# Kernel tuning notes

Measured on AMD Instinct MI355X. Metric: run time of the kernel, lower is better.

## Reference

```python
import jax, jax.numpy as jnp
import numpy as np

C = 1024
T = 2048
B = 8

def setup_inputs() -> dict:
    key = jax.random.key(0)
    ks = jax.random.split(key, 7)
    s = lambda fan_in: 1.0 / np.sqrt(fan_in)
    return {
        "x":     jax.random.normal(ks[0], (B, T, C), dtype=jnp.float32),
        "w_qkv": jax.random.uniform(ks[1], (C, 3 * C), jnp.float32, -s(C), s(C)),
        "w_proj": jax.random.uniform(ks[2], (C, C), jnp.float32, -s(C), s(C)),
        "w1":    jax.random.uniform(ks[3], (C, 2 * C), jnp.float32, -s(C), s(C)),
        "w2":    jax.random.uniform(ks[4], (2 * C, C), jnp.float32, -s(2 * C), s(2 * C)),
        "g1":    jnp.ones((C,), jnp.float32),
        "g2":    jnp.ones((C,), jnp.float32),
    }

def rmsnorm(x, g, eps=1e-6):
    return x * jax.lax.rsqrt(jnp.mean(x * x, axis=-1, keepdims=True) + eps) * g

def reference(x, w_qkv, w_proj, w1, w2, g1, g2):
    t = x.shape[1]
    # --- attention ---
    h = rmsnorm(x, g1)
    qkv = h @ w_qkv                               # [B,T,3C]
    q, k, v = jnp.split(qkv, 3, axis=-1)
    scores = jnp.einsum('bqc,bkc->bqk', q, k) * (C ** -0.5)  # [B,T,T]
    causal = jnp.triu(jnp.ones((t, t), dtype=bool), k=1)
    scores = jnp.where(causal, -jnp.inf, scores)
    attn = jax.nn.softmax(scores, axis=-1)
    x = x + (attn @ v) @ w_proj
    # --- ffn ---
    h = rmsnorm(x, g2)
    return x + (jax.nn.silu(h @ w1)) @ w2
```

## Files before the change

kernel.cpp:

```cpp
#include <hip/hip_runtime.h>
#include <hip/hip_bf16.h>
#include <stdint.h>


#define C_DIM 1024
#define T_DIM 2048
#define B_DIM 8

typedef float f32x4 __attribute__((ext_vector_type(4)));
typedef __bf16 bf16x8 __attribute__((ext_vector_type(8)));

typedef const __attribute__((address_space(1))) void gvoid_t;
typedef __attribute__((address_space(3))) void lvoid_t;

__device__ __forceinline__ void gload_lds16(const void* g, void* l) {
    __builtin_amdgcn_global_load_lds((gvoid_t*)g, (lvoid_t*)l, 16, 0, 0);
}

__device__ __forceinline__ unsigned short f2bf_bits(float f) {
    __hip_bfloat16 h = __float2bfloat16(f);
    return *reinterpret_cast<unsigned short*>(&h);
}

__device__ __forceinline__ void xcd_remap(int& bx, int& by, int& bz) {
    const int gx = gridDim.x, gy = gridDim.y;
    const int nwg = gx * gy * (int)gridDim.z;
    const int orig = bx + gx * (by + gy * bz);
    const int q = nwg >> 3, r = nwg & 7;
    const int xcd = orig & 7, pos = orig >> 3;
    const int neu = (xcd < r ? xcd * (q + 1) : r * (q + 1) + (xcd - r) * q) + pos;
    bx = neu % gx;
    const int t = neu / gx;
    by = t % gy;
    bz = t / gy;
}

#define BAR() do { __builtin_amdgcn_s_barrier(); __builtin_amdgcn_sched_barrier(0); } while(0)
#define VMCNT(n) do { asm volatile("s_waitcnt vmcnt(" #n ")" ::: "memory"); \
                      __builtin_amdgcn_sched_barrier(0); } while(0)

#define RD_A(dst, buf, hq) do { \
    _Pragma("unroll") \
    for (int mf_ = 0; mf_ < 4; ++mf_) { \
        const char* p_ = lds + (buf)*32768 + wrb + (hq)*8192 + mf_*2048; \
        dst[mf_][0] = *(const bf16x8*)(p_ + offk0); \
        dst[mf_][1] = *(const bf16x8*)(p_ + offk1); \
    } \
} while(0)

#define RD_B(dst, buf, nh) do { \
    _Pragma("unroll") \
    for (int n2_ = 0; n2_ < 2; ++n2_) { \
        const char* p_ = lds + 65536 + (buf)*32768 + wcb + ((nh)*2 + n2_)*2048; \
        dst[n2_][0] = *(const bf16x8*)(p_ + offk0); \
        dst[n2_][1] = *(const bf16x8*)(p_ + offk1); \
    } \
} while(0)

#define MMQ(aS, bS, Mh, Nh) do { \
    __builtin_amdgcn_s_setprio(1); \
    _Pragma("unroll") \
    for (int m4_ = 0; m4_ < 4; ++m4_) \
    _Pragma("unroll") \
    for (int n2_ = 0; n2_ < 2; ++n2_) \
    _Pragma("unroll") \
    for (int ks_ = 0; ks_ < 2; ++ks_) \
        acc[(Mh)*4 + m4_][(Nh)*2 + n2_] = __builtin_amdgcn_mfma_f32_16x16x32_bf16( \
            aS[m4_][ks_], bS[n2_][ks_], acc[(Mh)*4 + m4_][(Nh)*2 + n2_], 0, 0, 0); \
    __builtin_amdgcn_s_setprio(0); \
} while(0)

#define STA(buf, half, kt) do { \
    const int go_ = aoff + (half)*128*lda + (kt)*64; \
    char* lp_ = ldsw + (buf)*32768 + (half)*16384; \
    gload_lds16(A + go_,            lp_); \
    gload_lds16(A + go_ + 64*lda,   lp_ + 8192); \
} while(0)
#define STB(buf, half, kt) do { \
    const int go_ = boff + (half)*128*ldb + (kt)*64; \
    char* lp_ = ldsw + 65536 + (buf)*32768 + (half)*16384; \
    gload_lds16(Bt + go_,           lp_); \
    gload_lds16(Bt + go_ + 64*ldb,  lp_ + 8192); \
} while(0)
#define STAGE4(buf, kt) do { STA(buf,0,kt); STA(buf,1,kt); STB(buf,0,kt); STB(buf,1,kt); } while(0)

template<int EPI, int CMODE>
__global__ __launch_bounds__(512, 2)
void gemm256(const __hip_bfloat16* A, const __hip_bfloat16* Bt,
             void* Cout, const float* R, void* C2, void* C3,
             int K, int lda, int ldb, int ldc,
             long long sA, long long sB, long long sC, float scale)
{
    int bx = blockIdx.x, by = blockIdx.y, bz = blockIdx.z;
    xcd_remap(bx, by, bz);
    if constexpr (CMODE == 1) { if (bx > by) return; }

    const int tid  = threadIdx.x;
    const int lane = tid & 63, wave = tid >> 6;
    const int l15  = lane & 15, l4 = lane >> 4;
    const int wr   = wave >> 2, wc = wave & 3;
    const int m0   = by * 256, n0 = bx * 256;
    const int z    = bz;

    A  += (long long)z * sA;
    Bt += (long long)z * sB;

    __shared__ __align__(16) char lds_[131072];
    char* lds  = lds_;
    char* ldsw = lds_ + wave * 1024;

    int kmax = K;
    if constexpr (CMODE == 2) { int km = m0 + 256; kmax = km < K ? km : K; }
    const int NT = kmax >> 6, niter = NT >> 1;

    const int offk0 = l15 * 128 + (((l4)     ^ (l15 & 7)) << 4);
    const int offk1 = l15 * 128 + (((4 + l4) ^ (l15 & 7)) << 4);
    const int wrb = wr * 16384, wcb = wc * 8192;

    const int rowq  = tid >> 3;
    const int sslot = (tid & 7) ^ (rowq & 7);
    const int aoff  = (m0 + rowq) * lda + sslot * 8;
    const int boff  = (n0 + rowq) * ldb + sslot * 8;

    f32x4 acc[8][4];
#pragma unroll
    for (int i = 0; i < 8; ++i)
#pragma unroll
        for (int j = 0; j < 4; ++j) acc[i][j] = (f32x4){0.f, 0.f, 0.f, 0.f};
    bf16x8 aP[4][2], aQ[4][2], bL[2][2], bH[2][2];

    STAGE4(0, 0);
    STAGE4(1, 1);
    VMCNT(8);
    BAR();
    RD_A(aP, 0, 0);
    RD_B(bL, 0, 0);

    for (int it = 0; it < niter; ++it) {
        const int t0 = 2 * it, t1 = 2 * it + 1;
        RD_B(bH, 0, 1);            MMQ(aP, bL, 0, 0);
        RD_A(aQ, 0, 1);            MMQ(aP, bH, 0, 1);
                                   MMQ(aQ, bL, 1, 0);
        VMCNT(0); BAR();
        if (t0 + 2 < NT) STAGE4(0, t0 + 2);
        RD_A(aP, 1, 0);
        RD_B(bL, 1, 0);
                                   MMQ(aQ, bH, 1, 1);
        RD_B(bH, 1, 1);            MMQ(aP, bL, 0, 0);
        RD_A(aQ, 1, 1);            MMQ(aP, bH, 0, 1);
                                   MMQ(aQ, bL, 1, 0);
        VMCNT(0); BAR();
        if (t1 + 2 < NT) STAGE4(1, t1 + 2);
        if (it + 1 < niter) {
            RD_A(aP, 0, 0);
            RD_B(bL, 0, 0);
        }
                                   MMQ(aQ, bH, 1, 1);
    }

    asm volatile("s_waitcnt vmcnt(0)" ::: "memory");

    const long long cbase = (long long)z * sC;
#pragma unroll
    for (int mf = 0; mf < 8; ++mf) {
        const int rbase = m0 + wr * 128 + mf * 16 + l4 * 4;
#pragma unroll
        for (int nf = 0; nf < 4; ++nf) {
            const int col = n0 + wc * 64 + nf * 16 + l15;
#pragma unroll
            for (int r = 0; r < 4; ++r) {
                const float v = acc[mf][nf][r];
                const int row = rbase + r;
                if constexpr (EPI == 6) {
                    const int seg = col >> 10, ncol = col & 1023;
                    if (seg == 0) {
                        ((__hip_bfloat16*)Cout)[(long long)row * 1024 + ncol] =
                            __float2bfloat16(v);
                    } else if (seg == 1) {
                        ((__hip_bfloat16*)C2)[(long long)row * 1024 + ncol] =
                            __float2bfloat16(v);
                    } else {
                        const int b = row >> 11, t = row & 2047;
                        ((__hip_bfloat16*)C3)[((long long)b * C_DIM + ncol) * T_DIM + t] =
                            __float2bfloat16(v);
                    }
                } else {
                    const long long idx = cbase + (long long)row * ldc + col;
                    if constexpr (EPI == 0) {
                        ((__hip_bfloat16*)Cout)[idx] = __float2bfloat16(v);
                    } else if constexpr (EPI == 2) {
                        ((float*)Cout)[idx] = v + R[idx];
                    } else if constexpr (EPI == 3) {
                        const float s = v / (1.f + __expf(-v));
                        ((__hip_bfloat16*)Cout)[idx] = __float2bfloat16(s);
                    } else {
                        ((__hip_bfloat16*)Cout)[idx] = __float2bfloat16(v * scale);
                    }
                }
            }
        }
    }
}

__global__ __launch_bounds__(256)
void rmsnorm_kernel(const float* __restrict__ x, const float* __restrict__ g,
                    __hip_bfloat16* __restrict__ out)
{
    const long long row = blockIdx.x;
    const int tid = threadIdx.x;
    const float4 v = ((const float4*)(x + row * C_DIM))[tid];
    float ss = v.x * v.x + v.y * v.y + v.z * v.z + v.w * v.w;
#pragma unroll
    for (int off = 32; off; off >>= 1) ss += __shfl_xor(ss, off);
    __shared__ float red[4];
    if ((tid & 63) == 0) red[tid >> 6] = ss;
    __syncthreads();
    ss = red[0] + red[1] + red[2] + red[3];
    const float sc = rsqrtf(ss * (1.0f / C_DIM) + 1e-6f);
    const float4 gv = ((const float4*)g)[tid];
    ushort4 u;
    u.x = f2bf_bits(v.x * sc * gv.x);
    u.y = f2bf_bits(v.y * sc * gv.y);
    u.z = f2bf_bits(v.z * sc * gv.z);
    u.w = f2bf_bits(v.w * sc * gv.w);
    *(ushort4*)(out + row * C_DIM + tid * 4) = u;
}

__global__ __launch_bounds__(256)
void softmax_causal(__hip_bfloat16* __restrict__ SP)
{
    const int i = blockIdx.x, b = blockIdx.y;
    __hip_bfloat16* row = SP + ((long long)b * T_DIM + i) * T_DIM;
    const int tid = threadIdx.x;
    const int jbase = tid * 8;

    uint4 raw = ((const uint4*)row)[tid];
    float v[8];
    const unsigned w[4] = {raw.x, raw.y, raw.z, raw.w};
#pragma unroll
    for (int c = 0; c < 4; ++c) {
        unsigned lo = w[c] << 16;
        unsigned hi = w[c] & 0xFFFF0000u;
        v[2 * c]     = __uint_as_float(lo);
        v[2 * c + 1] = __uint_as_float(hi);
    }
#pragma unroll
    for (int e = 0; e < 8; ++e)
        if (jbase + e > i) v[e] = -1e30f;

    float m = v[0];
#pragma unroll
    for (int e = 1; e < 8; ++e) m = fmaxf(m, v[e]);
#pragma unroll
    for (int off = 32; off; off >>= 1) m = fmaxf(m, __shfl_xor(m, off));
    __shared__ float redm[4], reds[4];
    if ((tid & 63) == 0) redm[tid >> 6] = m;
    __syncthreads();
    m = fmaxf(fmaxf(redm[0], redm[1]), fmaxf(redm[2], redm[3]));

    float e8[8];
    float s = 0.f;
#pragma unroll
    for (int e = 0; e < 8; ++e) { e8[e] = __expf(v[e] - m); s += e8[e]; }
#pragma unroll
    for (int off = 32; off; off >>= 1) s += __shfl_xor(s, off);
    if ((tid & 63) == 0) reds[tid >> 6] = s;
    __syncthreads();
    s = reds[0] + reds[1] + reds[2] + reds[3];
    const float inv = 1.f / s;

    uint4 outw;
    unsigned o[4];
#pragma unroll
    for (int c = 0; c < 4; ++c) {
        unsigned lo = f2bf_bits(e8[2 * c] * inv);
        unsigned hi = f2bf_bits(e8[2 * c + 1] * inv);
        o[c] = lo | (hi << 16);
    }
    outw.x = o[0]; outw.y = o[1]; outw.z = o[2]; outw.w = o[3];
    ((uint4*)row)[tid] = outw;
}

__global__ __launch_bounds__(256)
void wcast_t(const float* __restrict__ in, __hip_bfloat16* __restrict__ out,
             int K, int N)
{
    __shared__ float t[32][33];
    const int n0 = blockIdx.x * 32, k0 = blockIdx.y * 32;
    const int tx = threadIdx.x, ty = threadIdx.y;
#pragma unroll
    for (int r = ty; r < 32; r += 8)
        t[r][tx] = in[(long long)(k0 + r) * N + n0 + tx];
    __syncthreads();
#pragma unroll
    for (int r = ty; r < 32; r += 8)
        out[(long long)(n0 + r) * K + k0 + tx] = __float2bfloat16(t[tx][r]);
}

extern "C" void kernel_launch(void* const* d_in, const int* in_sizes, int n_in,
                              void* d_out, int out_size, void* d_ws, size_t ws_size,
                              hipStream_t stream)
{
    const float* x      = (const float*)d_in[0];
    const float* w_qkv  = (const float*)d_in[1];
    const float* w_proj = (const float*)d_in[2];
    const float* w1     = (const float*)d_in[3];
    const float* w2     = (const float*)d_in[4];
    const float* g1     = (const float*)d_in[5];
    const float* g2     = (const float*)d_in[6];
    float* out = (float*)d_out;
    char* ws = (char*)d_ws;

    const size_t SP_off = 0;
    const size_t h_off  = 0;
    const size_t u_off  = 0;
    const size_t q_off  = 67108864ull;
    const size_t k_off  = 100663296ull;
    const size_t vT_off = 134217728ull;
    const size_t wq_off = 167772160ull;
    const size_t wp_off = wq_off + 6291456ull;
    const size_t w1_off = wp_off + 2097152ull;
    const size_t w2_off = w1_off + 4194304ull;
    const size_t NEED   = w2_off + 4194304ull;

    if (ws_size < NEED) return;

    auto bf = [&](size_t off) { return (__hip_bfloat16*)(ws + off); };

    wcast_t<<<dim3(96, 32), dim3(32, 8), 0, stream>>>(w_qkv,  bf(wq_off), 1024, 3072);
    wcast_t<<<dim3(32, 32), dim3(32, 8), 0, stream>>>(w_proj, bf(wp_off), 1024, 1024);
    wcast_t<<<dim3(64, 32), dim3(32, 8), 0, stream>>>(w1,     bf(w1_off), 1024, 2048);
    wcast_t<<<dim3(32, 64), dim3(32, 8), 0, stream>>>(w2,     bf(w2_off), 2048, 1024);

    rmsnorm_kernel<<<16384, 256, 0, stream>>>(x, g1, bf(h_off));

    gemm256<6, 0><<<dim3(12, 64, 1), 512, 0, stream>>>(
        bf(h_off), bf(wq_off), bf(q_off), nullptr, bf(k_off), bf(vT_off),
        1024, 1024, 1024, 1024, 0, 0, 0, 1.f);

    gemm256<4, 1><<<dim3(8, 8, 8), 512, 0, stream>>>(
        bf(q_off), bf(k_off), bf(SP_off), nullptr, nullptr, nullptr,
        1024, 1024, 1024, 2048,
        (long long)T_DIM * C_DIM, (long long)T_DIM * C_DIM, (long long)T_DIM * T_DIM,
        0.03125f);

    softmax_causal<<<dim3(2048, 8), 256, 0, stream>>>(bf(SP_off));

    gemm256<0, 2><<<dim3(4, 8, 8), 512, 0, stream>>>(
        bf(SP_off), bf(vT_off), bf(k_off) , nullptr, nullptr, nullptr,
        2048, 2048, 2048, 1024,
        (long long)T_DIM * T_DIM, (long long)C_DIM * T_DIM, (long long)T_DIM * C_DIM,
        1.f);

    gemm256<2, 0><<<dim3(4, 64, 1), 512, 0, stream>>>(
        bf(k_off) , bf(wp_off), out, x, nullptr, nullptr,
        1024, 1024, 1024, 1024, 0, 0, 0, 1.f);

    rmsnorm_kernel<<<16384, 256, 0, stream>>>(out, g2, bf(q_off));

    gemm256<3, 0><<<dim3(8, 64, 1), 512, 0, stream>>>(
        bf(q_off), bf(w1_off), bf(u_off), nullptr, nullptr, nullptr,
        1024, 1024, 1024, 2048, 0, 0, 0, 1.f);

    gemm256<2, 0><<<dim3(4, 64, 1), 512, 0, stream>>>(
        bf(u_off), bf(w2_off), out, (const float*)out, nullptr, nullptr,
        2048, 2048, 2048, 1024, 0, 0, 0, 1.f);
}
```

Measured before the change: 569.6 us.

## Restructure GEMM K-loop into barrier-phased per-quadrant schedule with split prefetch

Replaces the two-tile unrolled main loop of the 256x256 bf16 GEMM with a per-tile body split into four MMA quadrants. Each quadrant is separated by workgroup barriers and an explicit LDS wait, and the B and A prefetches for tile t+2 are interleaved between phases. The aim is a ping-pong style schedule where co-resident workgroups alternate memory and MFMA phases. It adds many barriers and removes the in-wave overlap of LDS reads with MFMAs, which may stall waves.

Result: slower. 596.2 us (+4.7%).

```diff
diff --git a/kernel.cpp b/kernel.cpp
--- a/kernel.cpp
+++ b/kernel.cpp
@@ -38,6 +38,8 @@
 #define BAR() do { __builtin_amdgcn_s_barrier(); __builtin_amdgcn_sched_barrier(0); } while(0)
 #define VMCNT(n) do { asm volatile("s_waitcnt vmcnt(" #n ")" ::: "memory"); \
                       __builtin_amdgcn_sched_barrier(0); } while(0)
+#define LGKM0() do { asm volatile("s_waitcnt lgkmcnt(0)" ::: "memory"); \
+                     __builtin_amdgcn_sched_barrier(0); } while(0)
 
 #define RD_A(dst, buf, hq) do { \
     _Pragma("unroll") \
@@ -82,7 +84,27 @@
     gload_lds16(Bt + go_,           lp_); \
     gload_lds16(Bt + go_ + 64*ldb,  lp_ + 8192); \
 } while(0)
-#define STAGE4(buf, kt) do { STA(buf,0,kt); STA(buf,1,kt); STB(buf,0,kt); STB(buf,1,kt); } while(0)
+
+#define TILE_BODY(t, STG) do { \
+    const int buf_ = (t) & 1; \
+     \
+    RD_B(bL, buf_, 0); \
+    BAR(); LGKM0(); MMQ(aX, bL, 0, 0); BAR(); \
+     \
+    if (STG) STB(buf_, 0, (t) + 2); \
+    RD_B(bH, buf_, 1); \
+    BAR(); LGKM0(); MMQ(aX, bH, 0, 1); BAR(); \
+     \
+    if (STG) STB(buf_, 1, (t) + 2); \
+    RD_A(aY, buf_, 1); \
+    BAR(); LGKM0(); MMQ(aY, bH, 1, 1); \
+    if (STG) { VMCNT(4); } else { VMCNT(0); } \
+    BAR(); \
+     \
+    if (STG) { STA(buf_, 0, (t) + 2); STA(buf_, 1, (t) + 2); } \
+    if ((t) + 1 < NT) RD_A(aX, buf_ ^ 1, 0); \
+    BAR(); LGKM0(); MMQ(aY, bL, 1, 0); BAR(); \
+} while(0)
 
 template<int EPI, int CMODE>
 __global__ __launch_bounds__(512, 2)
@@ -111,7 +133,7 @@
 
     int kmax = K;
     if constexpr (CMODE == 2) { int km = m0 + 256; kmax = km < K ? km : K; }
-    const int NT = kmax >> 6, niter = NT >> 1;
+    const int NT = kmax >> 6;
 
     const int offk0 = l15 * 128 + (((l4)     ^ (l15 & 7)) << 4);
     const int offk1 = l15 * 128 + (((4 + l4) ^ (l15 & 7)) << 4);
@@ -127,36 +149,17 @@
     for (int i = 0; i < 8; ++i)
 #pragma unroll
         for (int j = 0; j < 4; ++j) acc[i][j] = (f32x4){0.f, 0.f, 0.f, 0.f};
-    bf16x8 aP[4][2], aQ[4][2], bL[2][2], bH[2][2];
-
-    STAGE4(0, 0);
-    STAGE4(1, 1);
+    bf16x8 aX[4][2], aY[4][2], bL[2][2], bH[2][2];
+
+    STB(0, 0, 0); STB(0, 1, 0); STA(0, 0, 0); STA(0, 1, 0);
+    STB(1, 0, 1); STB(1, 1, 1); STA(1, 0, 1); STA(1, 1, 1);
     VMCNT(8);
     BAR();
-    RD_A(aP, 0, 0);
-    RD_B(bL, 0, 0);
-
-    for (int it = 0; it < niter; ++it) {
-        const int t0 = 2 * it, t1 = 2 * it + 1;
-        RD_B(bH, 0, 1);            MMQ(aP, bL, 0, 0);
-        RD_A(aQ, 0, 1);            MMQ(aP, bH, 0, 1);
-                                   MMQ(aQ, bL, 1, 0);
-        VMCNT(0); BAR();
-        if (t0 + 2 < NT) STAGE4(0, t0 + 2);
-        RD_A(aP, 1, 0);
-        RD_B(bL, 1, 0);
-                                   MMQ(aQ, bH, 1, 1);
-        RD_B(bH, 1, 1);            MMQ(aP, bL, 0, 0);
-        RD_A(aQ, 1, 1);            MMQ(aP, bH, 0, 1);
-                                   MMQ(aQ, bL, 1, 0);
-        VMCNT(0); BAR();
-        if (t1 + 2 < NT) STAGE4(1, t1 + 2);
-        if (it + 1 < niter) {
-            RD_A(aP, 0, 0);
-            RD_B(bL, 0, 0);
-        }
-                                   MMQ(aQ, bH, 1, 1);
-    }
+    RD_A(aX, 0, 0);
+
+    int t = 0;
+    for (; t < NT - 2; ++t) TILE_BODY(t, true);
+    for (; t < NT; ++t)     TILE_BODY(t, false);
 
     asm volatile("s_waitcnt vmcnt(0)" ::: "memory");
 
@@ -180,8 +183,8 @@
                         ((__hip_bfloat16*)C2)[(long long)row * 1024 + ncol] =
                             __float2bfloat16(v);
                     } else {
-                        const int b = row >> 11, t = row & 2047;
-                        ((__hip_bfloat16*)C3)[((long long)b * C_DIM + ncol) * T_DIM + t] =
+                        const int b = row >> 11, tt = row & 2047;
+                        ((__hip_bfloat16*)C3)[((long long)b * C_DIM + ncol) * T_DIM + tt] =
                             __float2bfloat16(v);
                     }
                 } else {
```
